# Kernel optimization log

Measured on AMD Instinct MI355X. Metric: run time of the kernel, lower is better.

Reference implementation:

```python
import math
import jax, jax.numpy as jnp
import numpy as np

NUM_HEAD = 16

def get_slopes(n):
    def pow2(n):
        start = 2 ** (-(2 ** (-(math.log2(n) - 3))))
        return [start * start ** i for i in range(n)]
    if math.log2(n).is_integer():
        return pow2(n)
    c = 2 ** math.floor(math.log2(n))
    return pow2(c) + get_slopes(2 * c)[0::2][: n - c]

def setup_inputs() -> dict:
    key = jax.random.key(0)
    ks = jax.random.split(key, 5)
    B, T, D = 2, 2048, 1024
    x = jax.random.normal(ks[0], (B, T, D), dtype=jnp.float32)
    Wq = jax.random.normal(ks[1], (D, D), dtype=jnp.float32) * 0.02
    Wk = jax.random.normal(ks[2], (D, D), dtype=jnp.float32) * 0.02
    Wv = jax.random.normal(ks[3], (D, D), dtype=jnp.float32) * 0.02
    Wo = jax.random.normal(ks[4], (D, D), dtype=jnp.float32) * (0.02 / math.sqrt(2 * 24))
    return {"x": x, "Wq": Wq, "Wk": Wk, "Wv": Wv, "Wo": Wo}

def reference(x, Wq, Wk, Wv, Wo):
    B, T, D = x.shape
    H = NUM_HEAD
    hd = D // H
    # projections (no bias)
    q = (x @ Wq).reshape(B, T, H, hd).transpose(0, 2, 1, 3)  # b h t d
    k = (x @ Wk).reshape(B, T, H, hd).transpose(0, 2, 1, 3)
    v = (x @ Wv).reshape(B, T, H, hd).transpose(0, 2, 1, 3)
    scores = jnp.einsum("bhqd,bhkd->bhqk", q, k) / jnp.sqrt(jnp.asarray(hd, dtype=q.dtype))
    # ALiBi bias: slopes[h] * (j - (T-1)), broadcast over query positions
    slopes = jnp.asarray(np.array(get_slopes(H), dtype=np.float32))
    alibi = slopes[:, None, None] * (jnp.arange(T, dtype=jnp.float32) - (T - 1))[None, None, :]  # h 1 k
    scores = scores + alibi[None]  # b h q k
    causal = jnp.tril(jnp.ones((T, T), dtype=bool))
    masked = jnp.where(causal[None, None], scores.astype(jnp.float32), jnp.finfo(jnp.float32).min)
    p = jax.nn.softmax(masked, axis=-1)
    attn_out = jnp.einsum("bhqk,bhkd->bhqd", p, v)
    attn_out = attn_out.transpose(0, 2, 1, 3).reshape(B, T, D)
    return attn_out @ Wo
```

## Files before the change

### kernel.cpp

```cpp
#include <hip/hip_runtime.h>
#include <hip/hip_bf16.h>
#include <math.h>

#define B_ 2
#define T_ 2048
#define D_ 1024
#define H_ 16
#define HD 64

typedef __bf16 bf16;
typedef bf16 bf16x8 __attribute__((ext_vector_type(8)));
typedef bf16 bf16x4 __attribute__((ext_vector_type(4)));
typedef short short4v __attribute__((ext_vector_type(4)));
typedef float f32x4 __attribute__((ext_vector_type(4)));

#define GL2LDS16(g, l) __builtin_amdgcn_global_load_lds(                      \
    (const __attribute__((address_space(1))) void*)(g),                       \
    (__attribute__((address_space(3))) void*)(l), 16, 0, 0)

static __device__ __forceinline__ f32x4 mfma16x16x16(bf16x4 a, bf16x4 b, f32x4 c) {
#if defined(__HIP_DEVICE_COMPILE__)
# if __has_builtin(__builtin_amdgcn_mfma_f32_16x16x16bf16_1k)
    return __builtin_amdgcn_mfma_f32_16x16x16bf16_1k(
        __builtin_bit_cast(short4v, a), __builtin_bit_cast(short4v, b), c, 0, 0, 0);
# else
    asm("v_mfma_f32_16x16x16_bf16 %0, %1, %2, %0" : "+v"(c) : "v"(a), "v"(b));
    return c;
# endif
#else
    (void)a; (void)b;
    return c;
#endif
}

__global__ __launch_bounds__(256) void prep_inputs(const float* __restrict__ x,
                                                   const float* __restrict__ W0,
                                                   const float* __restrict__ W1,
                                                   const float* __restrict__ W2,
                                                   const float* __restrict__ W3,
                                                   bf16* __restrict__ xb,
                                                   bf16* __restrict__ Wt) {
    const int z = blockIdx.z;
    const int tid = threadIdx.x;
    if (z >= 4) {
        size_t i = ((((size_t)(z - 4) * 256 + blockIdx.y * 16 + blockIdx.x) * 256) + tid) * 4;
        float4 v = *(const float4*)(x + i);
        bf16 tmp[4] = {(bf16)v.x, (bf16)v.y, (bf16)v.z, (bf16)v.w};
        *(uint2*)(xb + i) = *(const uint2*)tmp;
        return;
    }
    __shared__ bf16 tile[64 * 72];
    const float* W = (z == 0) ? W0 : (z == 1) ? W1 : (z == 2) ? W2 : W3;
    bf16* out = Wt + (size_t)z * D_ * D_;
    const int k0 = blockIdx.y * 64, n0 = blockIdx.x * 64;
    for (int it = 0; it < 4; ++it) {
        int idx = it * 256 + tid;
        int r = idx >> 4;
        int c4 = (idx & 15) << 2;
        float4 v = *(const float4*)(W + (size_t)(k0 + r) * D_ + n0 + c4);
        tile[(c4 + 0) * 72 + r] = (bf16)v.x;
        tile[(c4 + 1) * 72 + r] = (bf16)v.y;
        tile[(c4 + 2) * 72 + r] = (bf16)v.z;
        tile[(c4 + 3) * 72 + r] = (bf16)v.w;
    }
    __syncthreads();
    for (int it = 0; it < 2; ++it) {
        int idx = it * 256 + tid;
        int r = idx >> 3;
        int c8 = (idx & 7) << 3;
        bf16x8 v = *(const bf16x8*)&tile[r * 72 + c8];
        *(bf16x8*)(out + (size_t)(n0 + r) * D_ + k0 + c8) = v;
    }
}

__global__ __launch_bounds__(256) void gemm_bf16(const bf16* __restrict__ A,
                                                 const bf16* __restrict__ Bt,
                                                 void* __restrict__ Cout,
                                                 int M, int N, int K, int mode) {
    __shared__ bf16 As[2][128 * 32];
    __shared__ bf16 Bs[2][64 * 32];
    const int tid = threadIdx.x;
    const int wave = tid >> 6, lane = tid & 63;
    const int quad = lane >> 4, l16 = lane & 15;
    const int wr = wave >> 1, wc = wave & 1;
    const int m0 = blockIdx.y * 128, n0 = blockIdx.x * 64;
    const int z = blockIdx.z;
    const bf16* Bz = Bt + (size_t)z * N * K;
    const bool swapped = (mode == 1) || (z < 2);

    const int lrow = lane >> 2, lcol = (lane & 3) << 3;
    const bf16* ag = A  + (size_t)(m0 + wave * 32 + lrow) * K + lcol;
    const bf16* bg = Bz + (size_t)(n0 + wave * 16 + lrow) * K + lcol;
    const int a_off = (wave * 32 + lrow) * 32 + lcol;
    const int b_off = (wave * 16 + lrow) * 32 + lcol;

    f32x4 acc[4][2];
    for (int mi = 0; mi < 4; ++mi)
        for (int ni = 0; ni < 2; ++ni) acc[mi][ni] = (f32x4){0.f, 0.f, 0.f, 0.f};

    for (int kb = 0; kb < K; kb += 64) {
        GL2LDS16(ag + kb,                       &As[0][a_off]);
        GL2LDS16(ag + (size_t)16 * K + kb,      &As[0][a_off + 16 * 32]);
        GL2LDS16(ag + kb + 32,                  &As[1][a_off]);
        GL2LDS16(ag + (size_t)16 * K + kb + 32, &As[1][a_off + 16 * 32]);
        GL2LDS16(bg + kb,                       &Bs[0][b_off]);
        GL2LDS16(bg + kb + 32,                  &Bs[1][b_off]);
        __syncthreads();

        for (int half = 0; half < 2; ++half) {
            bf16x8 af[4], bfr[2];
            for (int mi = 0; mi < 4; ++mi)
                af[mi] = *(const bf16x8*)&As[half][(wr * 64 + mi * 16 + l16) * 32 + quad * 8];
            for (int ni = 0; ni < 2; ++ni)
                bfr[ni] = *(const bf16x8*)&Bs[half][(wc * 32 + ni * 16 + l16) * 32 + quad * 8];
            if (swapped) {
                for (int mi = 0; mi < 4; ++mi)
                    for (int ni = 0; ni < 2; ++ni)
                        acc[mi][ni] = __builtin_amdgcn_mfma_f32_16x16x32_bf16(
                            bfr[ni], af[mi], acc[mi][ni], 0, 0, 0);
            } else {
                for (int mi = 0; mi < 4; ++mi)
                    for (int ni = 0; ni < 2; ++ni)
                        acc[mi][ni] = __builtin_amdgcn_mfma_f32_16x16x32_bf16(
                            af[mi], bfr[ni], acc[mi][ni], 0, 0, 0);
            }
        }
        __syncthreads();
    }

    if (mode == 0) {
        bf16* Cb = (bf16*)Cout + (size_t)z * M * N;
        if (z < 2) {
            for (int mi = 0; mi < 4; ++mi)
                for (int ni = 0; ni < 2; ++ni) {
                    int m = m0 + wr * 64 + mi * 16 + l16;
                    int n = n0 + wc * 32 + ni * 16 + quad * 4;
                    int b = m >> 11, t = m & (T_ - 1);
                    int h = n >> 6, d = n & (HD - 1);
                    bf16 o4[4];
                    for (int r = 0; r < 4; ++r) o4[r] = (bf16)acc[mi][ni][r];
                    *(uint2*)&Cb[(((((size_t)b * H_ + h) * T_ + t) << 6) + d)] =
                        *(const uint2*)o4;
                }
        } else {
            for (int mi = 0; mi < 4; ++mi)
                for (int ni = 0; ni < 2; ++ni) {
                    int m = m0 + wr * 64 + mi * 16 + quad * 4;
                    int n = n0 + wc * 32 + ni * 16 + l16;
                    int b = m >> 11, t = m & (T_ - 1);
                    int h = n >> 6, d = n & (HD - 1);
                    bf16 o4[4];
                    for (int r = 0; r < 4; ++r) o4[r] = (bf16)acc[mi][ni][r];
                    *(uint2*)&Cb[((((size_t)b * H_ + h) * HD + d) * T_ + t)] =
                        *(const uint2*)o4;
                }
        }
    } else {
        float* Cf = (float*)Cout;
        for (int mi = 0; mi < 4; ++mi)
            for (int ni = 0; ni < 2; ++ni) {
                int m = m0 + wr * 64 + mi * 16 + l16;
                int n = n0 + wc * 32 + ni * 16 + quad * 4;
                *(f32x4*)&Cf[(size_t)m * N + n] = acc[mi][ni];
            }
    }
}

__device__ __constant__ unsigned char ITEM_QT[48] = {
    14,15,16,17,18,19,20,21,22,23,24,25,26,27,28,29,30,31,30,31,
    12,13,28,29, 10,11,26,27, 8,9,24,25, 6,7,22,23,
    4,5,20,21, 2,3,18,19, 0,1,16,17};
__device__ __constant__ unsigned char ITEM_KIND[48] = {
    0,0,1,1,1,1,1,1,1,1,1,1,1,1,1,1,1,1,2,2,
    0,0,2,2, 0,0,2,2, 0,0,2,2, 0,0,2,2,
    0,0,2,2, 0,0,2,2, 0,0,2,2};

#define LDK 72
#define LDP 136

__global__ __launch_bounds__(256, 4) void attn_kernel(const bf16* __restrict__ Q,
                                                      const bf16* __restrict__ K,
                                                      const bf16* __restrict__ Vt,
                                                      bf16* __restrict__ O,
                                                      float* __restrict__ Opart,
                                                      float2* __restrict__ ML) {
    __shared__ bf16 Ks[128 * LDK];
    __shared__ bf16 Vs[64 * LDP];

    const int bh = blockIdx.x;
    const int item = blockIdx.y;
    const int qt = ITEM_QT[item];
    const int kind = ITEM_KIND[item];
    const int h = bh & (H_ - 1), b = bh >> 4;
    const int tid = threadIdx.x;
    const int wave = tid >> 6, lane = tid & 63;
    const int quad = lane >> 4, l16 = lane & 15;

    const bf16* Qb = Q + (size_t)bh * T_ * HD;
    const bf16* Kb = K + (size_t)bh * T_ * HD;
    const bf16* Vb = Vt + (size_t)bh * HD * T_;

    const float LOG2E = 1.44269504f;
    const float slope2 = exp2f(-0.5f * (float)(h + 1)) * LOG2E;
    const float c1 = 0.125f * LOG2E;

    bf16x8 qf[2];
    {
        const bf16* qrow = Qb + (size_t)(qt * 64 + wave * 16 + l16) * HD + quad * 8;
        qf[0] = *(const bf16x8*)(qrow);
        qf[1] = *(const bf16x8*)(qrow + 32);
    }

    f32x4 acc[4];
    for (int df = 0; df < 4; ++df) acc[df] = (f32x4){0.f, 0.f, 0.f, 0.f};
    float m_run = -INFINITY, l_run = 0.f;

    const int qglob = qt * 64 + wave * 16 + l16;
    const int nkt = (qt >> 1) + 1;
    const int kt0 = (kind == 2) ? 8 : 0;
    const int kt1 = (kind == 1) ? 8 : nkt;

    for (int kt = kt0; kt < kt1; ++kt) {
        const bool last = (kt == nkt - 1);
        __syncthreads();
        for (int it = 0; it < 4; ++it) {
            int idx = it * 256 + tid;
            int rk = idx >> 3, ck = (idx & 7) << 3;
            *(bf16x8*)&Ks[rk * LDK + ck] =
                *(const bf16x8*)(Kb + (size_t)(kt * 128 + rk) * HD + ck);
            int rv = idx >> 4, cv = (idx & 15) << 3;
            *(bf16x8*)&Vs[rv * LDP + cv] =
                *(const bf16x8*)(Vb + (size_t)rv * T_ + kt * 128 + cv);
        }
        __syncthreads();

        f32x4 s[8];
        for (int nf = 0; nf < 8; ++nf) {
            bf16x8 kf0 = *(const bf16x8*)&Ks[(nf * 16 + l16) * LDK + quad * 8];
            bf16x8 kf1 = *(const bf16x8*)&Ks[(nf * 16 + l16) * LDK + 32 + quad * 8];
            f32x4 zz = (f32x4){0.f, 0.f, 0.f, 0.f};
            zz = __builtin_amdgcn_mfma_f32_16x16x32_bf16(kf0, qf[0], zz, 0, 0, 0);
            zz = __builtin_amdgcn_mfma_f32_16x16x32_bf16(kf1, qf[1], zz, 0, 0, 0);
            s[nf] = zz;
        }

        const int jbase = kt * 128 + quad * 4;
        for (int nf = 0; nf < 8; ++nf)
            for (int r = 0; r < 4; ++r) {
                int j = jbase + nf * 16 + r;
                s[nf][r] = s[nf][r] * c1 + slope2 * (float)(j - (T_ - 1));
            }
        if (last) {
            for (int nf = 0; nf < 8; ++nf)
                for (int r = 0; r < 4; ++r)
                    if (jbase + nf * 16 + r > qglob) s[nf][r] = -INFINITY;
        }

        float mx = -INFINITY;
        for (int nf = 0; nf < 8; ++nf) {
            float a = fmaxf(fmaxf(s[nf][0], s[nf][1]), fmaxf(s[nf][2], s[nf][3]));
            mx = fmaxf(mx, a);
        }
        mx = fmaxf(mx, __shfl_xor(mx, 16, 64));
        mx = fmaxf(mx, __shfl_xor(mx, 32, 64));
        const float mnew = fmaxf(m_run, mx);
        const float alpha = exp2f(m_run - mnew);
        m_run = mnew;

        float rs = 0.f;
        bf16x4 pf[8];
        for (int nf = 0; nf < 8; ++nf) {
            float p0 = exp2f(s[nf][0] - mnew);
            float p1 = exp2f(s[nf][1] - mnew);
            float p2 = exp2f(s[nf][2] - mnew);
            float p3 = exp2f(s[nf][3] - mnew);
            rs += (p0 + p1) + (p2 + p3);
            pf[nf] = (bf16x4){(bf16)p0, (bf16)p1, (bf16)p2, (bf16)p3};
        }
        rs += __shfl_xor(rs, 16, 64);
        rs += __shfl_xor(rs, 32, 64);
        l_run = l_run * alpha + rs;
        for (int df = 0; df < 4; ++df) acc[df] *= alpha;

        for (int nf = 0; nf < 8; ++nf)
            for (int df = 0; df < 4; ++df) {
                bf16x4 vf = *(const bf16x4*)&Vs[(df * 16 + l16) * LDP + nf * 16 + quad * 4];
                acc[df] = mfma16x16x16(vf, pf[nf], acc[df]);
            }
    }

    if (kind == 0) {
        const float inv = 1.0f / l_run;
        for (int df = 0; df < 4; ++df) {
            bf16 o4[4];
            for (int r = 0; r < 4; ++r) o4[r] = (bf16)(acc[df][r] * inv);
            *(uint2*)&O[(((size_t)b * T_ + qglob) * H_ + h) * HD + df * 16 + quad * 4] =
                *(const uint2*)o4;
        }
    } else {
        const int pidx = (bh * 16 + (qt - 16)) * 2 + (kind == 2 ? 1 : 0);
        const int ql = wave * 16 + l16;
        float* dst = Opart + (size_t)pidx * 4096 + ql * 64;
        for (int df = 0; df < 4; ++df)
            *(f32x4*)&dst[df * 16 + quad * 4] = acc[df];
        if (quad == 0) ML[pidx * 64 + ql] = make_float2(m_run, l_run);
    }
}

__global__ __launch_bounds__(256) void attn_merge(const float* __restrict__ Opart,
                                                  const float2* __restrict__ ML,
                                                  bf16* __restrict__ O) {
    const int qt = 16 + blockIdx.x, bh = blockIdx.y;
    const int h = bh & (H_ - 1), b = bh >> 4;
    const int tid = threadIdx.x;
    const int q = tid >> 2, dc = (tid & 3) << 4;
    const int p0 = (bh * 16 + blockIdx.x) * 2, p1 = p0 + 1;

    const float2 ml0 = ML[p0 * 64 + q], ml1 = ML[p1 * 64 + q];
    const float M = fmaxf(ml0.x, ml1.x);
    const float e0 = exp2f(ml0.x - M), e1 = exp2f(ml1.x - M);
    const float inv = 1.0f / (e0 * ml0.y + e1 * ml1.y);

    const float* a = Opart + (size_t)p0 * 4096 + q * 64 + dc;
    const float* c = Opart + (size_t)p1 * 4096 + q * 64 + dc;
    bf16 o16[16];
    for (int j = 0; j < 4; ++j) {
        f32x4 va = *(const f32x4*)(a + j * 4);
        f32x4 vc = *(const f32x4*)(c + j * 4);
        for (int r = 0; r < 4; ++r)
            o16[j * 4 + r] = (bf16)((va[r] * e0 + vc[r] * e1) * inv);
    }
    const int t = qt * 64 + q;
    bf16* dst = O + (((size_t)b * T_ + t) * H_ + h) * HD + dc;
    *(bf16x8*)dst = *(const bf16x8*)o16;
    *(bf16x8*)(dst + 8) = *(const bf16x8*)(o16 + 8);
}

extern "C" void kernel_launch(void* const* d_in, const int* in_sizes, int n_in,
                              void* d_out, int out_size, void* d_ws, size_t ws_size,
                              hipStream_t stream) {
    const float* x  = (const float*)d_in[0];
    const float* Wq = (const float*)d_in[1];
    const float* Wk = (const float*)d_in[2];
    const float* Wv = (const float*)d_in[3];
    const float* Wo = (const float*)d_in[4];
    float* out = (float*)d_out;

    const size_t M = (size_t)B_ * T_;
    const size_t XE = M * D_;
    const size_t WE = (size_t)D_ * D_;

    char* ws = (char*)d_ws;
    size_t off = 0;
    auto carve = [&](size_t bytes) {
        void* p = ws + off;
        off += (bytes + 255) & ~(size_t)255;
        return p;
    };
    bf16* xb  = (bf16*)carve(XE * 2);
    bf16* Wt  = (bf16*)carve(4 * WE * 2);
    bf16* QKV = (bf16*)carve(3 * XE * 2);
    float*  Opart = (float*)carve(32 * 16 * 2 * 4096 * sizeof(float));
    float2* MLbuf = (float2*)carve(32 * 16 * 2 * 64 * sizeof(float2));
    bf16* attn = xb;

    prep_inputs<<<dim3(16, 16, 20), 256, 0, stream>>>(x, Wq, Wk, Wv, Wo, xb, Wt);

    gemm_bf16<<<dim3(D_ / 64, M / 128, 3), 256, 0, stream>>>(xb, Wt, QKV,
                                                             (int)M, D_, D_, 0);
    attn_kernel<<<dim3(32, 48), 256, 0, stream>>>(QKV, QKV + XE, QKV + 2 * XE,
                                                  attn, Opart, MLbuf);
    attn_merge<<<dim3(16, 32), 256, 0, stream>>>(Opart, MLbuf, attn);
    gemm_bf16<<<dim3(D_ / 64, M / 128, 1), 256, 0, stream>>>(attn, Wt + 3 * WE, out,
                                                             (int)M, D_, D_, 1);
}
```

Before: 210.5 us.

## Double-buffer GEMM LDS tiles to overlap global loads with MFMA compute

The bf16 GEMM's shared-memory tiles gain a second buffer. The next K-block is now loaded with global_load_lds while MFMAs run on the current buffer, instead of loading and synchronizing before every block. Explicit s_waitcnt vmcnt and s_barrier replace __syncthreads so the prefetched loads can stay in flight. This doubles LDS use per block, which may lower occupancy, and depends on the hand-written wait counts staying correct.

New measurement: 212.4 us. Within noise of the previous version (+0.9%).

```diff
diff --git a/kernel.cpp b/kernel.cpp
--- a/kernel.cpp
+++ b/kernel.cpp
@@ -77,8 +77,8 @@
                                                  const bf16* __restrict__ Bt,
                                                  void* __restrict__ Cout,
                                                  int M, int N, int K, int mode) {
-    __shared__ bf16 As[2][128 * 32];
-    __shared__ bf16 Bs[2][64 * 32];
+    __shared__ bf16 As[2][2][128 * 32];
+    __shared__ bf16 Bs[2][2][64 * 32];
     const int tid = threadIdx.x;
     const int wave = tid >> 6, lane = tid & 63;
     const int quad = lane >> 4, l16 = lane & 15;
@@ -98,21 +98,33 @@
     for (int mi = 0; mi < 4; ++mi)
         for (int ni = 0; ni < 2; ++ni) acc[mi][ni] = (f32x4){0.f, 0.f, 0.f, 0.f};
 
-    for (int kb = 0; kb < K; kb += 64) {
-        GL2LDS16(ag + kb,                       &As[0][a_off]);
-        GL2LDS16(ag + (size_t)16 * K + kb,      &As[0][a_off + 16 * 32]);
-        GL2LDS16(ag + kb + 32,                  &As[1][a_off]);
-        GL2LDS16(ag + (size_t)16 * K + kb + 32, &As[1][a_off + 16 * 32]);
-        GL2LDS16(bg + kb,                       &Bs[0][b_off]);
-        GL2LDS16(bg + kb + 32,                  &Bs[1][b_off]);
-        __syncthreads();
+    auto issue = [&](int kb, int buf) {
+        GL2LDS16(ag + kb,                       &As[buf][0][a_off]);
+        GL2LDS16(ag + (size_t)16 * K + kb,      &As[buf][0][a_off + 16 * 32]);
+        GL2LDS16(ag + kb + 32,                  &As[buf][1][a_off]);
+        GL2LDS16(ag + (size_t)16 * K + kb + 32, &As[buf][1][a_off + 16 * 32]);
+        GL2LDS16(bg + kb,                       &Bs[buf][0][b_off]);
+        GL2LDS16(bg + kb + 32,                  &Bs[buf][1][b_off]);
+    };
+
+    issue(0, 0);
+    const int niter = K >> 6;
+    for (int it = 0; it < niter; ++it) {
+        const int cur = it & 1;
+        if (it + 1 < niter) {
+            issue((it + 1) << 6, cur ^ 1);
+            asm volatile("s_waitcnt vmcnt(6)" ::: "memory");
+        } else {
+            asm volatile("s_waitcnt vmcnt(0)" ::: "memory");
+        }
+        asm volatile("s_barrier" ::: "memory");
 
         for (int half = 0; half < 2; ++half) {
             bf16x8 af[4], bfr[2];
             for (int mi = 0; mi < 4; ++mi)
-                af[mi] = *(const bf16x8*)&As[half][(wr * 64 + mi * 16 + l16) * 32 + quad * 8];
+                af[mi] = *(const bf16x8*)&As[cur][half][(wr * 64 + mi * 16 + l16) * 32 + quad * 8];
             for (int ni = 0; ni < 2; ++ni)
-                bfr[ni] = *(const bf16x8*)&Bs[half][(wc * 32 + ni * 16 + l16) * 32 + quad * 8];
+                bfr[ni] = *(const bf16x8*)&Bs[cur][half][(wc * 32 + ni * 16 + l16) * 32 + quad * 8];
             if (swapped) {
                 for (int mi = 0; mi < 4; ++mi)
                     for (int ni = 0; ni < 2; ++ni)
@@ -125,7 +137,7 @@
                             af[mi], bfr[ni], acc[mi][ni], 0, 0, 0);
             }
         }
-        __syncthreads();
+        asm volatile("s_barrier" ::: "memory");
     }
 
     if (mode == 0) {
```
